# Performance work log

Hardware: AMD Instinct MI355X
Metric: run time of the kernel (lower is better)

## Reference

```python
import jax, jax.numpy as jnp
import numpy as np

# dims
B, T, D, H, A = 256, 64, 6400, 1000, 4
# config['snn'] / config['adaptive_threshold'] values
BETA = 0.9          # 1 - voltage_decay(0.1)
THRESH = 1.0        # threshold_voltage
REST = 0.0          # resting_voltage
THETA_PLUS = 0.05
THETA_DECAY = 0.9


def setup_inputs() -> dict:
    key = jax.random.key(0)
    ks = jax.random.split(key, 7)
    x = jax.random.normal(ks[0], (B, T, D), jnp.float32)
    W1 = jax.random.normal(ks[1], (H, D), jnp.float32) * (1.0 / np.sqrt(D))
    b1 = jax.random.normal(ks[2], (H,), jnp.float32) * 0.01
    W2 = jax.random.normal(ks[3], (A, H), jnp.float32) * (1.0 / np.sqrt(H))
    b2 = jax.random.normal(ks[4], (A,), jnp.float32) * 0.01
    # pre-drawn uniforms for bernoulli sampling at each timestep/layer
    u1 = jax.random.uniform(ks[5], (T, B, H), jnp.float32)
    u2 = jax.random.uniform(ks[6], (T, B, A), jnp.float32)
    return {"x": x, "W1": W1, "b1": b1, "W2": W2, "b2": b2, "u1": u1, "u2": u2}


def _lif(cur, mem, theta, u):
    # StochasticAdaptiveLIF.forward
    mem = BETA * (mem - REST) + REST + cur
    prob = jax.nn.sigmoid(mem - (THRESH + theta))
    spk = (u < prob).astype(mem.dtype)  # bernoulli(prob)
    mem = mem * (1.0 - spk)
    theta = THETA_DECAY * theta + THETA_PLUS * spk
    return spk, mem, theta


def reference(x, W1, b1, W2, b2, u1, u2):
    xT = jnp.swapaxes(x, 0, 1)  # [T, B, D]

    def step(carry, inp):
        mem1, theta1, mem2, theta2 = carry
        xt, u1t, u2t = inp
        cur1 = xt @ W1.T + b1                      # [B, H]
        spk1, mem1, theta1 = _lif(cur1, mem1, theta1, u1t)
        cur2 = spk1 @ W2.T + b2                    # [B, A]
        spk2, mem2, theta2 = _lif(cur2, mem2, theta2, u2t)
        return (mem1, theta1, mem2, theta2), spk2

    init = (jnp.zeros((B, H), x.dtype), jnp.zeros((B, H), x.dtype),
            jnp.zeros((B, A), x.dtype), jnp.zeros((B, A), x.dtype))
    _, spks = jax.lax.scan(step, init, (xT, u1, u2))  # spks: [T, B, A]
    return spks.sum(0) / T
```

## Files before the change

### kernel.cpp

```cpp
#include <hip/hip_runtime.h>
#include <math.h>

#define B_  256
#define T_  64
#define D_  6400
#define H_  1000
#define A_  4

#define BM 128
#define BN 128
#define BK 16

__global__ __launch_bounds__(256) void gemm1_kernel(
    const float* __restrict__ x, const float* __restrict__ W1,
    const float* __restrict__ b1, float* __restrict__ C1) {
  __shared__ float As[BK][BM + 4];
  __shared__ float Bs[BK][BN + 4];

  const int tid = threadIdx.x;
  const int m0 = blockIdx.y * BM;
  const int n0 = blockIdx.x * BN;
  const int tx = tid & 15;
  const int ty = tid >> 4;

  const int row = tid >> 2;
  const int col4 = tid & 3;

  float acc[8][8];
#pragma unroll
  for (int i = 0; i < 8; ++i)
#pragma unroll
    for (int j = 0; j < 8; ++j) acc[i][j] = 0.0f;

  float4 av[2], bv[2];
#pragma unroll
  for (int i = 0; i < 2; ++i) {
    const int r = row + 64 * i;
    av[i] = *(const float4*)(x + (size_t)(m0 + r) * D_ + col4 * 4);
    const int h = n0 + r;
    bv[i] = (h < H_) ? *(const float4*)(W1 + (size_t)h * D_ + col4 * 4)
                     : make_float4(0.f, 0.f, 0.f, 0.f);
  }

  for (int k0 = 0; k0 < D_; k0 += BK) {
    __syncthreads();
#pragma unroll
    for (int i = 0; i < 2; ++i) {
      const int r = row + 64 * i;
      As[col4 * 4 + 0][r] = av[i].x;
      As[col4 * 4 + 1][r] = av[i].y;
      As[col4 * 4 + 2][r] = av[i].z;
      As[col4 * 4 + 3][r] = av[i].w;
      Bs[col4 * 4 + 0][r] = bv[i].x;
      Bs[col4 * 4 + 1][r] = bv[i].y;
      Bs[col4 * 4 + 2][r] = bv[i].z;
      Bs[col4 * 4 + 3][r] = bv[i].w;
    }
    __syncthreads();
    if (k0 + BK < D_) {
      const int kn = k0 + BK;
#pragma unroll
      for (int i = 0; i < 2; ++i) {
        const int r = row + 64 * i;
        av[i] = *(const float4*)(x + (size_t)(m0 + r) * D_ + kn + col4 * 4);
        const int h = n0 + r;
        bv[i] = (h < H_) ? *(const float4*)(W1 + (size_t)h * D_ + kn + col4 * 4)
                         : make_float4(0.f, 0.f, 0.f, 0.f);
      }
    }
#pragma unroll
    for (int k = 0; k < BK; ++k) {
      const float4 a0 = *(const float4*)&As[k][ty * 4];
      const float4 a1 = *(const float4*)&As[k][64 + ty * 4];
      const float4 b0 = *(const float4*)&Bs[k][tx * 4];
      const float4 b1v = *(const float4*)&Bs[k][64 + tx * 4];
      const float ar[8] = {a0.x, a0.y, a0.z, a0.w, a1.x, a1.y, a1.z, a1.w};
      const float br[8] = {b0.x, b0.y, b0.z, b0.w, b1v.x, b1v.y, b1v.z, b1v.w};
#pragma unroll
      for (int i = 0; i < 8; ++i)
#pragma unroll
        for (int j = 0; j < 8; ++j) acc[i][j] = fmaf(ar[i], br[j], acc[i][j]);
    }
  }

  const int h0 = n0 + tx * 4;
  const int h1 = n0 + 64 + tx * 4;
  float4 bias0 = (h0 < H_) ? *(const float4*)(b1 + h0)
                           : make_float4(0.f, 0.f, 0.f, 0.f);
  float4 bias1 = (h1 < H_) ? *(const float4*)(b1 + h1)
                           : make_float4(0.f, 0.f, 0.f, 0.f);
#pragma unroll
  for (int ih = 0; ih < 2; ++ih) {
#pragma unroll
    for (int i2 = 0; i2 < 4; ++i2) {
      const int i = ih * 4 + i2;
      const int m = m0 + ih * 64 + ty * 4 + i2;
      const int bb = m >> 6;
      const int tt = m & 63;
      float* op = C1 + (size_t)tt * (B_ * H_) + (size_t)bb * H_;
      if (h0 < H_) {
        float4 r0;
        r0.x = acc[i][0] + bias0.x;
        r0.y = acc[i][1] + bias0.y;
        r0.z = acc[i][2] + bias0.z;
        r0.w = acc[i][3] + bias0.w;
        *(float4*)(op + h0) = r0;
      }
      if (h1 < H_) {
        float4 r1;
        r1.x = acc[i][4] + bias1.x;
        r1.y = acc[i][5] + bias1.y;
        r1.z = acc[i][6] + bias1.z;
        r1.w = acc[i][7] + bias1.w;
        *(float4*)(op + h1) = r1;
      }
    }
  }
}

__device__ __forceinline__ float sigmoid_f(float z) {
  return 1.0f / (1.0f + expf(-z));
}

__global__ __launch_bounds__(256) void snn_seq_kernel(
    const float* __restrict__ C1, const float* __restrict__ u1,
    const float* __restrict__ W2, const float* __restrict__ b2,
    const float* __restrict__ u2, float* __restrict__ out) {
  const int b = blockIdx.x;
  const int tid = threadIdx.x;
  const int lane = tid & 63;
  const int wv = tid >> 6;

  __shared__ float sW2[A_ * H_];
  __shared__ float sRed[4][A_];

  for (int i = tid; i < A_ * H_; i += 256) sW2[i] = W2[i];
  __syncthreads();

  float mem1[4] = {0.f, 0.f, 0.f, 0.f};
  float th1[4] = {0.f, 0.f, 0.f, 0.f};
  float mem2[A_] = {0.f, 0.f, 0.f, 0.f};
  float th2[A_] = {0.f, 0.f, 0.f, 0.f};
  float scnt[A_] = {0.f, 0.f, 0.f, 0.f};

  for (int t = 0; t < T_; ++t) {
    const float* c1p = C1 + (size_t)t * (B_ * H_) + (size_t)b * H_;
    const float* u1p = u1 + (size_t)t * (B_ * H_) + (size_t)b * H_;
    float part[A_] = {0.f, 0.f, 0.f, 0.f};
#pragma unroll
    for (int k = 0; k < 4; ++k) {
      const int h = k * 256 + tid;
      if (h < H_) {
        const float cur = c1p[h];
        float m = fmaf(0.9f, mem1[k], cur);
        const float z = m - (1.0f + th1[k]);
        const float p = sigmoid_f(z);
        const float spk = (u1p[h] < p) ? 1.0f : 0.0f;
        m = (spk != 0.0f) ? 0.0f : m;
        th1[k] = fmaf(0.9f, th1[k], 0.05f * spk);
        mem1[k] = m;
        if (spk != 0.0f) {
          part[0] += sW2[h];
          part[1] += sW2[H_ + h];
          part[2] += sW2[2 * H_ + h];
          part[3] += sW2[3 * H_ + h];
        }
      }
    }
#pragma unroll
    for (int off = 32; off >= 1; off >>= 1) {
#pragma unroll
      for (int a = 0; a < A_; ++a) part[a] += __shfl_down(part[a], off);
    }
    if (lane == 0) {
      sRed[wv][0] = part[0];
      sRed[wv][1] = part[1];
      sRed[wv][2] = part[2];
      sRed[wv][3] = part[3];
    }
    __syncthreads();
    if (tid == 0) {
#pragma unroll
      for (int a = 0; a < A_; ++a) {
        const float cur2 =
            sRed[0][a] + sRed[1][a] + sRed[2][a] + sRed[3][a] + b2[a];
        float m = fmaf(0.9f, mem2[a], cur2);
        const float z = m - (1.0f + th2[a]);
        const float p = sigmoid_f(z);
        const float u = u2[(size_t)t * (B_ * A_) + b * A_ + a];
        const float spk = (u < p) ? 1.0f : 0.0f;
        mem2[a] = (spk != 0.0f) ? 0.0f : m;
        th2[a] = fmaf(0.9f, th2[a], 0.05f * spk);
        scnt[a] += spk;
      }
    }
    __syncthreads();
  }

  if (tid == 0) {
#pragma unroll
    for (int a = 0; a < A_; ++a) out[b * A_ + a] = scnt[a] * (1.0f / 64.0f);
  }
}

extern "C" void kernel_launch(void* const* d_in, const int* in_sizes, int n_in,
                              void* d_out, int out_size, void* d_ws,
                              size_t ws_size, hipStream_t stream) {
  const float* x = (const float*)d_in[0];
  const float* W1 = (const float*)d_in[1];
  const float* b1 = (const float*)d_in[2];
  const float* W2 = (const float*)d_in[3];
  const float* b2 = (const float*)d_in[4];
  const float* u1 = (const float*)d_in[5];
  const float* u2 = (const float*)d_in[6];
  float* out = (float*)d_out;
  float* C1 = (float*)d_ws;

  dim3 g1((H_ + BN - 1) / BN, (B_ * T_) / BM);
  gemm1_kernel<<<g1, 256, 0, stream>>>(x, W1, b1, C1);
  snn_seq_kernel<<<B_, 256, 0, stream>>>(C1, u1, W2, b2, u2, out);
}
```

Measured before the change: 3.216 ms.

## Enlarge GEMM M-tile to 256 and use packed FP32 FMA via inline asm

Doubles the M tile of the first GEMM so each thread computes a 16x8 output block, raising arithmetic intensity per shared-memory load and reusing each W1 tile across more rows. The inner product is rewritten with v_pk_fma_f32 inline assembly, using op_sel to broadcast one A element across a pair of B elements, so each instruction does two FMAs. The larger accumulator array raises register pressure, and launch bounds now request two blocks per CU. Grid block count halves, which may reduce occupancy and load balance.

```diff
diff --git a/kernel.cpp b/kernel.cpp
--- a/kernel.cpp
+++ b/kernel.cpp
@@ -7,11 +7,22 @@
 #define H_  1000
 #define A_  4
 
-#define BM 128
+#define BM 256
 #define BN 128
 #define BK 16
 
-__global__ __launch_bounds__(256) void gemm1_kernel(
+typedef float v2f __attribute__((ext_vector_type(2)));
+
+#define PK_FMA_LO(acc, a, b)                                          \
+  asm("v_pk_fma_f32 %0, %1, %2, %0 op_sel:[0,0,0] op_sel_hi:[0,1,1]" \
+      : "+v"(acc)                                                     \
+      : "v"(a), "v"(b))
+#define PK_FMA_HI(acc, a, b)                                          \
+  asm("v_pk_fma_f32 %0, %1, %2, %0 op_sel:[1,0,0] op_sel_hi:[1,1,1]" \
+      : "+v"(acc)                                                     \
+      : "v"(a), "v"(b))
+
+__global__ __launch_bounds__(256, 2) void gemm1_kernel(
     const float* __restrict__ x, const float* __restrict__ W1,
     const float* __restrict__ b1, float* __restrict__ C1) {
   __shared__ float As[BK][BM + 4];
@@ -26,18 +37,19 @@
   const int row = tid >> 2;
   const int col4 = tid & 3;
 
-  float acc[8][8];
-#pragma unroll
-  for (int i = 0; i < 8; ++i)
-#pragma unroll
-    for (int j = 0; j < 8; ++j) acc[i][j] = 0.0f;
-
-  float4 av[2], bv[2];
+  v2f acc2[16][4];
+#pragma unroll
+  for (int i = 0; i < 16; ++i)
+#pragma unroll
+    for (int j = 0; j < 4; ++j) acc2[i][j] = (v2f){0.f, 0.f};
+
+  float4 av[4], bv[2];
+#pragma unroll
+  for (int i = 0; i < 4; ++i)
+    av[i] = *(const float4*)(x + (size_t)(m0 + row + 64 * i) * D_ + col4 * 4);
 #pragma unroll
   for (int i = 0; i < 2; ++i) {
-    const int r = row + 64 * i;
-    av[i] = *(const float4*)(x + (size_t)(m0 + r) * D_ + col4 * 4);
-    const int h = n0 + r;
+    const int h = n0 + row + 64 * i;
     bv[i] = (h < H_) ? *(const float4*)(W1 + (size_t)h * D_ + col4 * 4)
                      : make_float4(0.f, 0.f, 0.f, 0.f);
   }
@@ -45,12 +57,16 @@
   for (int k0 = 0; k0 < D_; k0 += BK) {
     __syncthreads();
 #pragma unroll
-    for (int i = 0; i < 2; ++i) {
+    for (int i = 0; i < 4; ++i) {
       const int r = row + 64 * i;
       As[col4 * 4 + 0][r] = av[i].x;
       As[col4 * 4 + 1][r] = av[i].y;
       As[col4 * 4 + 2][r] = av[i].z;
       As[col4 * 4 + 3][r] = av[i].w;
+    }
+#pragma unroll
+    for (int i = 0; i < 2; ++i) {
+      const int r = row + 64 * i;
       Bs[col4 * 4 + 0][r] = bv[i].x;
       Bs[col4 * 4 + 1][r] = bv[i].y;
       Bs[col4 * 4 + 2][r] = bv[i].z;
@@ -60,26 +76,36 @@
     if (k0 + BK < D_) {
       const int kn = k0 + BK;
 #pragma unroll
+      for (int i = 0; i < 4; ++i)
+        av[i] =
+            *(const float4*)(x + (size_t)(m0 + row + 64 * i) * D_ + kn + col4 * 4);
+#pragma unroll
       for (int i = 0; i < 2; ++i) {
-        const int r = row + 64 * i;
-        av[i] = *(const float4*)(x + (size_t)(m0 + r) * D_ + kn + col4 * 4);
-        const int h = n0 + r;
-        bv[i] = (h < H_) ? *(const float4*)(W1 + (size_t)h * D_ + kn + col4 * 4)
-                         : make_float4(0.f, 0.f, 0.f, 0.f);
+        const int h = n0 + row + 64 * i;
+        bv[i] = (h < H_)
+                    ? *(const float4*)(W1 + (size_t)h * D_ + kn + col4 * 4)
+                    : make_float4(0.f, 0.f, 0.f, 0.f);
       }
     }
 #pragma unroll
     for (int k = 0; k < BK; ++k) {
       const float4 a0 = *(const float4*)&As[k][ty * 4];
       const float4 a1 = *(const float4*)&As[k][64 + ty * 4];
+      const float4 a2 = *(const float4*)&As[k][128 + ty * 4];
+      const float4 a3 = *(const float4*)&As[k][192 + ty * 4];
       const float4 b0 = *(const float4*)&Bs[k][tx * 4];
       const float4 b1v = *(const float4*)&Bs[k][64 + tx * 4];
-      const float ar[8] = {a0.x, a0.y, a0.z, a0.w, a1.x, a1.y, a1.z, a1.w};
-      const float br[8] = {b0.x, b0.y, b0.z, b0.w, b1v.x, b1v.y, b1v.z, b1v.w};
-#pragma unroll
-      for (int i = 0; i < 8; ++i)
-#pragma unroll
-        for (int j = 0; j < 8; ++j) acc[i][j] = fmaf(ar[i], br[j], acc[i][j]);
+      v2f ap[8] = {{a0.x, a0.y}, {a0.z, a0.w}, {a1.x, a1.y}, {a1.z, a1.w},
+                   {a2.x, a2.y}, {a2.z, a2.w}, {a3.x, a3.y}, {a3.z, a3.w}};
+      v2f bp[4] = {{b0.x, b0.y}, {b0.z, b0.w}, {b1v.x, b1v.y}, {b1v.z, b1v.w}};
+#pragma unroll
+      for (int p = 0; p < 8; ++p) {
+#pragma unroll
+        for (int j = 0; j < 4; ++j) {
+          PK_FMA_LO(acc2[2 * p][j], ap[p], bp[j]);
+          PK_FMA_HI(acc2[2 * p + 1][j], ap[p], bp[j]);
+        }
+      }
     }
   }
 
@@ -90,30 +116,26 @@
   float4 bias1 = (h1 < H_) ? *(const float4*)(b1 + h1)
                            : make_float4(0.f, 0.f, 0.f, 0.f);
 #pragma unroll
-  for (int ih = 0; ih < 2; ++ih) {
-#pragma unroll
-    for (int i2 = 0; i2 < 4; ++i2) {
-      const int i = ih * 4 + i2;
-      const int m = m0 + ih * 64 + ty * 4 + i2;
-      const int bb = m >> 6;
-      const int tt = m & 63;
-      float* op = C1 + (size_t)tt * (B_ * H_) + (size_t)bb * H_;
-      if (h0 < H_) {
-        float4 r0;
-        r0.x = acc[i][0] + bias0.x;
-        r0.y = acc[i][1] + bias0.y;
-        r0.z = acc[i][2] + bias0.z;
-        r0.w = acc[i][3] + bias0.w;
-        *(float4*)(op + h0) = r0;
-      }
-      if (h1 < H_) {
-        float4 r1;
-        r1.x = acc[i][4] + bias1.x;
-        r1.y = acc[i][5] + bias1.y;
-        r1.z = acc[i][6] + bias1.z;
-        r1.w = acc[i][7] + bias1.w;
-        *(float4*)(op + h1) = r1;
-      }
+  for (int f = 0; f < 16; ++f) {
+    const int m = m0 + 64 * (f >> 2) + ty * 4 + (f & 3);
+    const int bb = m >> 6;
+    const int tt = m & 63;
+    float* op = C1 + (size_t)tt * (B_ * H_) + (size_t)bb * H_;
+    if (h0 < H_) {
+      float4 r;
+      r.x = acc2[f][0].x + bias0.x;
+      r.y = acc2[f][0].y + bias0.y;
+      r.z = acc2[f][1].x + bias0.z;
+      r.w = acc2[f][1].y + bias0.w;
+      *(float4*)(op + h0) = r;
+    }
+    if (h1 < H_) {
+      float4 r;
+      r.x = acc2[f][2].x + bias1.x;
+      r.y = acc2[f][2].y + bias1.y;
+      r.z = acc2[f][3].x + bias1.z;
+      r.w = acc2[f][3].y + bias1.w;
+      *(float4*)(op + h1) = r;
     }
   }
 }
```

New measurement: 3.004 ms. -6.6%, faster.
